# Performance work log

Hardware: AMD Instinct MI355X
Metric: run time of the kernel (lower is better)

Reference implementation:

```python
import jax, jax.numpy as jnp
import numpy as np

EMBED_DIM = 512
NUM_HEADS = 8
N_WIRES = 8  # kernel uses only first N_WIRES dims of each head vector


def setup_inputs() -> dict:
    key = jax.random.key(0)
    x = jax.random.normal(key, (8, 1024, EMBED_DIM), dtype=jnp.float32)
    return {"x": x}


def reference(x):
    B, S, E = x.shape
    H = NUM_HEADS
    dk = E // H
    # [B, H, S, dk]
    xh = x.reshape(B, S, H, dk).transpose(0, 2, 1, 3)
    # Quantum RY-overlap kernel closed form:
    #   RY(-y) RY(x) |0> = RY(x - y) |0>  =>  <0...0|psi> = prod_w cos((x_w - y_w)/2)
    # Only the first N_WIRES components of each head vector are used
    # (states.view(-1)[0] reads the first batch row's |0..0> amplitude).
    xw = xh[..., :N_WIRES]  # [B, H, S, NW]
    scores = jnp.ones((B, H, S, S), dtype=x.dtype)
    for w in range(N_WIRES):  # fixed small loop, fuses under jit
        diff = xw[:, :, :, None, w] - xw[:, :, None, :, w]  # [B, H, S, S]
        scores = scores * jnp.cos(diff * 0.5)
    scores = jnp.abs(scores)
    attn = jax.nn.softmax(scores, axis=-1)  # dropout is identity at eval
    out = jnp.einsum("bhij,bhjd->bhid", attn, xh)  # [B, H, S, dk]
    return out.transpose(0, 2, 1, 3).reshape(B, S, E)
```

## Files before the change

kernel.cpp:

```cpp
#include <hip/hip_runtime.h>

#define B_  8
#define S_  1024
#define E_  512
#define TI  128
#define TJ  32
#define P_STR 40
#define V_STR 40

typedef _Float16 half_t;
typedef _Float16 half4_t __attribute__((ext_vector_type(4)));
typedef _Float16 half8_t __attribute__((ext_vector_type(8)));
typedef float    floatx16 __attribute__((ext_vector_type(16)));

__device__ __forceinline__ void make_frags(float4 w0, float4 w1, int hf,
                                           half8_t* fH, half8_t* fL) {
    float xi[8] = {w0.x, w0.y, w0.z, w0.w, w1.x, w1.y, w1.z, w1.w};
    float c[8], s[8];
    #pragma unroll
    for (int w = 0; w < 8; ++w) {
        float v = xi[w] * 0.5f;
        c[w] = __cosf(v);
        s[w] = __sinf(v);
    }
    float p01[4] = {c[0]*c[1], s[0]*c[1], c[0]*s[1], s[0]*s[1]};
    float p23[4] = {c[2]*c[3], s[2]*c[3], c[2]*s[3], s[2]*s[3]};
    float p45[4] = {c[4]*c[5], s[4]*c[5], c[4]*s[5], s[4]*s[5]};
    float p67[4] = {c[6]*c[7], s[6]*c[7], c[6]*s[7], s[6]*s[7]};
    #pragma unroll
    for (int idx = 0; idx < 8; ++idx) {
        int a = idx & 3;
        int bsel = (idx >> 2) | (hf << 1);
        (*fL)[idx] = (half_t)(p01[a] * p23[bsel]);
        (*fH)[idx] = (half_t)(p45[a] * p67[bsel]);
    }
}

__global__ __launch_bounds__(256, 2) void attn_kernel(const float* __restrict__ x,
                                                      float* __restrict__ out) {
    const int bh = blockIdx.x;
    const int b  = bh >> 3, h = bh & 7;
    const int i0 = blockIdx.y * TI;
    const int t  = threadIdx.x;
    const int wv = t >> 6;
    const int ln = t & 63;
    const int m  = ln & 31;
    const int hf = ln >> 5;
    const int lo = t & 7;

    __shared__ __align__(16) half_t sh_p[TI * P_STR];
    __shared__ __align__(16) half_t sh_v[64 * V_STR];
    __shared__ float sh_den[TI];

    const float* xh = x + (size_t)b * S_ * E_ + h * 64;

    half8_t biH, biL;
    {
        const float* px = xh + (size_t)(i0 + wv * 32 + m) * E_;
        float4 w0 = ((const float4*)px)[0];
        float4 w1 = ((const float4*)px)[1];
        make_frags(w0, w1, hf, &biH, &biL);
    }

    floatx16 acc0, acc1, z;
    #pragma unroll
    for (int k = 0; k < 16; ++k) { acc0[k] = 0.f; acc1[k] = 0.f; z[k] = 0.f; }
    float dacc = 0.f;

    const int sv_j  = t >> 3;
    const int sv_d0 = lo * 8;

    for (int j0 = 0; j0 < S_; j0 += TJ) {
        __syncthreads();

        const float* pj = xh + (size_t)(j0 + m) * E_;
        float4 jw0 = ((const float4*)pj)[0];
        float4 jw1 = ((const float4*)pj)[1];
        const float* pv = xh + (size_t)(j0 + sv_j) * E_ + sv_d0;
        float4 v0 = ((const float4*)pv)[0];
        float4 v1 = ((const float4*)pv)[1];

        half8_t ajH, ajL;
        make_frags(jw0, jw1, hf, &ajH, &ajL);

        {
            float vals[8] = {v0.x, v0.y, v0.z, v0.w, v1.x, v1.y, v1.z, v1.w};
            #pragma unroll
            for (int nq = 0; nq < 8; ++nq) {
                int q = (nq + lo) & 7;
                sh_v[(sv_d0 + q) * V_STR + sv_j] = (half_t)vals[q];
            }
        }
        __syncthreads();

        floatx16 sH = __builtin_amdgcn_mfma_f32_32x32x16_f16(ajH, biH, z, 0, 0, 0);
        floatx16 sL = __builtin_amdgcn_mfma_f32_32x32x16_f16(ajL, biL, z, 0, 0, 0);

        const int irow = wv * 32 + m;
        #pragma unroll
        for (int g = 0; g < 4; ++g) {
            half4_t pk;
            #pragma unroll
            for (int r = 0; r < 4; ++r) {
                float sc = sH[4 * g + r] * sL[4 * g + r];
                float p = __expf(__builtin_fabsf(sc));
                dacc += p;
                pk[r] = (half_t)p;
            }
            *(half4_t*)&sh_p[irow * P_STR + g * 8 + hf * 4] = pk;
        }

        const half_t* prow = &sh_p[(wv * 32 + m) * P_STR];
        half8_t ap0 = *(const half8_t*)(prow + hf * 8);
        half8_t ap1 = *(const half8_t*)(prow + 16 + hf * 8);
        const half_t* vr0 = &sh_v[m * V_STR];
        const half_t* vr1 = &sh_v[(32 + m) * V_STR];
        half8_t b00 = *(const half8_t*)(vr0 + hf * 8);
        half8_t b01 = *(const half8_t*)(vr0 + 16 + hf * 8);
        half8_t b10 = *(const half8_t*)(vr1 + hf * 8);
        half8_t b11 = *(const half8_t*)(vr1 + 16 + hf * 8);
        acc0 = __builtin_amdgcn_mfma_f32_32x32x16_f16(ap0, b00, acc0, 0, 0, 0);
        acc0 = __builtin_amdgcn_mfma_f32_32x32x16_f16(ap1, b01, acc0, 0, 0, 0);
        acc1 = __builtin_amdgcn_mfma_f32_32x32x16_f16(ap0, b10, acc1, 0, 0, 0);
        acc1 = __builtin_amdgcn_mfma_f32_32x32x16_f16(ap1, b11, acc1, 0, 0, 0);
    }

    dacc += __shfl_xor(dacc, 32, 64);
    sh_den[wv * 32 + m] = dacc;
    __syncthreads();

    #pragma unroll
    for (int reg = 0; reg < 16; ++reg) {
        int il = (reg & 3) + 8 * (reg >> 2) + 4 * hf;
        float inv = 1.f / sh_den[wv * 32 + il];
        size_t base = ((size_t)(b * S_ + i0 + wv * 32 + il)) * E_ + h * 64 + m;
        out[base]      = acc0[reg] * inv;
        out[base + 32] = acc1[reg] * inv;
    }
}

extern "C" void kernel_launch(void* const* d_in, const int* in_sizes, int n_in,
                              void* d_out, int out_size, void* d_ws, size_t ws_size,
                              hipStream_t stream) {
    const float* x = (const float*)d_in[0];
    float* out = (float*)d_out;
    attn_kernel<<<dim3(B_ * 8, S_ / TI), 256, 0, stream>>>(x, out);
}
```

Before: 112.1 us.

## Precompute fp16 feature maps and transposed V, split j across waves

Adds a precompute kernel that evaluates the cos/sin product feature vectors once per row and writes an fp16 transposed copy of V to workspace. The attention kernel then loads these directly, staging V with global_load_lds and skipping per-tile transcendental work and fp32 conversion. P fragments are built with permlane32 swaps instead of an LDS round trip. The tile becomes 64x64 with two waves splitting j and a shared-memory reduction at the end. This costs an extra launch and workspace traffic, and the j split adds an epilogue reduction.

```diff
diff --git a/kernel.cpp b/kernel.cpp
--- a/kernel.cpp
+++ b/kernel.cpp
@@ -3,139 +3,175 @@
 #define B_  8
 #define S_  1024
 #define E_  512
-#define TI  128
-#define TJ  32
-#define P_STR 40
-#define V_STR 40
+#define TI  64
+#define TJ  64
 
 typedef _Float16 half_t;
-typedef _Float16 half4_t __attribute__((ext_vector_type(4)));
+typedef _Float16 half2_t __attribute__((ext_vector_type(2)));
 typedef _Float16 half8_t __attribute__((ext_vector_type(8)));
 typedef float    floatx16 __attribute__((ext_vector_type(16)));
+typedef unsigned int uint2v __attribute__((ext_vector_type(2)));
+typedef unsigned int uint4v __attribute__((ext_vector_type(4)));
 
-__device__ __forceinline__ void make_frags(float4 w0, float4 w1, int hf,
-                                           half8_t* fH, half8_t* fL) {
-    float xi[8] = {w0.x, w0.y, w0.z, w0.w, w1.x, w1.y, w1.z, w1.w};
-    float c[8], s[8];
-    #pragma unroll
-    for (int w = 0; w < 8; ++w) {
-        float v = xi[w] * 0.5f;
-        c[w] = __cosf(v);
-        s[w] = __sinf(v);
+#define PHI_BYTES ((size_t)64 * S_ * 32 * 2)
+#define VT_BYTES  ((size_t)64 * 64 * S_ * 2)
+
+#define GLOAD_LDS16(g, l)                                                        \
+    __builtin_amdgcn_global_load_lds((const __attribute__((address_space(1))) void*)(g), \
+                                     (__attribute__((address_space(3))) void*)(l), 16, 0, 0)
+
+__global__ __launch_bounds__(256) void precompute_kernel(const float* __restrict__ x,
+                                                         half_t* __restrict__ phi,
+                                                         half_t* __restrict__ vt) {
+    const int bh  = blockIdx.y;
+    const int b   = bh >> 3, h = bh & 7;
+    const int jb0 = blockIdx.x * 128;
+    const int t   = threadIdx.x;
+    __shared__ half_t tsh[128 * 65];
+
+    {
+        const int jj = t >> 1, sel = t & 1;
+        const int j  = jb0 + jj;
+        const float* px = x + (size_t)b * S_ * E_ + (size_t)j * E_ + h * 64 + sel * 4;
+        float4 w = *(const float4*)px;
+        float xi[4] = {w.x, w.y, w.z, w.w};
+        float c[4], s[4];
+        #pragma unroll
+        for (int q = 0; q < 4; ++q) {
+            float v = xi[q] * 0.5f;
+            c[q] = __cosf(v); s[q] = __sinf(v);
+        }
+        float pa[4] = {c[0]*c[1], s[0]*c[1], c[0]*s[1], s[0]*s[1]};
+        float pb[4] = {c[2]*c[3], s[2]*c[3], c[2]*s[3], s[2]*s[3]};
+        half_t f16[16];
+        #pragma unroll
+        for (int f = 0; f < 16; ++f)
+            f16[f] = (half_t)(pa[f & 3] * pb[f >> 2]);
+        half_t* dst = phi + ((size_t)bh * S_ + j) * 32 + (sel ? 0 : 16);
+        *(half8_t*)dst       = *(half8_t*)&f16[0];
+        *(half8_t*)(dst + 8) = *(half8_t*)&f16[8];
     }
-    float p01[4] = {c[0]*c[1], s[0]*c[1], c[0]*s[1], s[0]*s[1]};
-    float p23[4] = {c[2]*c[3], s[2]*c[3], c[2]*s[3], s[2]*s[3]};
-    float p45[4] = {c[4]*c[5], s[4]*c[5], c[4]*s[5], s[4]*s[5]};
-    float p67[4] = {c[6]*c[7], s[6]*c[7], c[6]*s[7], s[6]*s[7]};
-    #pragma unroll
-    for (int idx = 0; idx < 8; ++idx) {
-        int a = idx & 3;
-        int bsel = (idx >> 2) | (hf << 1);
-        (*fL)[idx] = (half_t)(p01[a] * p23[bsel]);
-        (*fH)[idx] = (half_t)(p45[a] * p67[bsel]);
+
+    {
+        const float* xb = x + (size_t)b * S_ * E_ + h * 64;
+        for (int k = 0; k < 32; ++k) {
+            int idx = k * 256 + t;
+            int j = idx >> 6, d = idx & 63;
+            tsh[j * 65 + d] = (half_t)xb[(size_t)(jb0 + j) * E_ + d];
+        }
+        __syncthreads();
+        for (int k = 0; k < 32; ++k) {
+            int idx = k * 256 + t;
+            int d = idx >> 7, j = idx & 127;
+            vt[((size_t)bh * 64 + d) * S_ + jb0 + j] = tsh[j * 65 + d];
+        }
     }
 }
 
-__global__ __launch_bounds__(256, 2) void attn_kernel(const float* __restrict__ x,
+__global__ __launch_bounds__(256, 4) void attn_kernel(const half_t* __restrict__ phi,
+                                                      const half_t* __restrict__ vt,
                                                       float* __restrict__ out) {
-    const int bh = blockIdx.x;
-    const int b  = bh >> 3, h = bh & 7;
-    const int i0 = blockIdx.y * TI;
-    const int t  = threadIdx.x;
-    const int wv = t >> 6;
-    const int ln = t & 63;
-    const int m  = ln & 31;
-    const int hf = ln >> 5;
-    const int lo = t & 7;
+    const int iblk = blockIdx.x;
+    const int bh   = blockIdx.y;
+    const int b    = bh >> 3, h = bh & 7;
+    const int i0   = iblk * TI;
+    const int t    = threadIdx.x;
+    const int wv   = t >> 6, ln = t & 63;
+    const int m    = ln & 31, hf = ln >> 5;
+    const int ib   = wv >> 1, jb = wv & 1;
 
-    __shared__ __align__(16) half_t sh_p[TI * P_STR];
-    __shared__ __align__(16) half_t sh_v[64 * V_STR];
-    __shared__ float sh_den[TI];
+    __shared__ __align__(16) half_t sh_v[8 * 64 * 8];
+    __shared__ float sh_red[2][32][64];
+    __shared__ float sh_den[2][64];
 
-    const float* xh = x + (size_t)b * S_ * E_ + h * 64;
+    const half_t* phb = phi + (size_t)bh * S_ * 32;
 
     half8_t biH, biL;
     {
-        const float* px = xh + (size_t)(i0 + wv * 32 + m) * E_;
-        float4 w0 = ((const float4*)px)[0];
-        float4 w1 = ((const float4*)px)[1];
-        make_frags(w0, w1, hf, &biH, &biL);
+        const half_t* pr = phb + (size_t)(i0 + ib * 32 + m) * 32 + hf * 8;
+        biH = *(const half8_t*)pr;
+        biL = *(const half8_t*)(pr + 16);
     }
 
     floatx16 acc0, acc1, z;
     #pragma unroll
     for (int k = 0; k < 16; ++k) { acc0[k] = 0.f; acc1[k] = 0.f; z[k] = 0.f; }
-    float dacc = 0.f;
+    float d0 = 0.f, d1 = 0.f;
 
-    const int sv_j  = t >> 3;
-    const int sv_d0 = lo * 8;
+    const half_t* vsrc = vt + ((size_t)bh * 64 + ln) * S_;
+    const half_t* asrc = phb + (size_t)(jb * 32 + m) * 32 + hf * 8;
 
     for (int j0 = 0; j0 < S_; j0 += TJ) {
         __syncthreads();
 
-        const float* pj = xh + (size_t)(j0 + m) * E_;
-        float4 jw0 = ((const float4*)pj)[0];
-        float4 jw1 = ((const float4*)pj)[1];
-        const float* pv = xh + (size_t)(j0 + sv_j) * E_ + sv_d0;
-        float4 v0 = ((const float4*)pv)[0];
-        float4 v1 = ((const float4*)pv)[1];
+        GLOAD_LDS16(vsrc + j0 + (2 * wv + 0) * 8, &sh_v[(2 * wv + 0) * 64 * 8]);
+        GLOAD_LDS16(vsrc + j0 + (2 * wv + 1) * 8, &sh_v[(2 * wv + 1) * 64 * 8]);
 
-        half8_t ajH, ajL;
-        make_frags(jw0, jw1, hf, &ajH, &ajL);
-
-        {
-            float vals[8] = {v0.x, v0.y, v0.z, v0.w, v1.x, v1.y, v1.z, v1.w};
-            #pragma unroll
-            for (int nq = 0; nq < 8; ++nq) {
-                int q = (nq + lo) & 7;
-                sh_v[(sv_d0 + q) * V_STR + sv_j] = (half_t)vals[q];
-            }
-        }
-        __syncthreads();
+        const half_t* ar = asrc + (size_t)j0 * 32;
+        half8_t ajH = *(const half8_t*)ar;
+        half8_t ajL = *(const half8_t*)(ar + 16);
 
         floatx16 sH = __builtin_amdgcn_mfma_f32_32x32x16_f16(ajH, biH, z, 0, 0, 0);
         floatx16 sL = __builtin_amdgcn_mfma_f32_32x32x16_f16(ajL, biL, z, 0, 0, 0);
 
-        const int irow = wv * 32 + m;
+        unsigned int dwa[4], dwb[4];
         #pragma unroll
         for (int g = 0; g < 4; ++g) {
-            half4_t pk;
+            float p[4];
             #pragma unroll
             for (int r = 0; r < 4; ++r) {
                 float sc = sH[4 * g + r] * sL[4 * g + r];
-                float p = __expf(__builtin_fabsf(sc));
-                dacc += p;
-                pk[r] = (half_t)p;
+                p[r] = __expf(__builtin_fabsf(sc));
             }
-            *(half4_t*)&sh_p[irow * P_STR + g * 8 + hf * 4] = pk;
+            d0 += p[0] + p[2];
+            d1 += p[1] + p[3];
+            half2_t ha = {(half_t)p[0], (half_t)p[1]};
+            half2_t hb = {(half_t)p[2], (half_t)p[3]};
+            dwa[g] = __builtin_bit_cast(unsigned int, ha);
+            dwb[g] = __builtin_bit_cast(unsigned int, hb);
         }
+        uint2v swA0 = __builtin_amdgcn_permlane32_swap(dwa[0], dwa[1], false, false);
+        uint2v swB0 = __builtin_amdgcn_permlane32_swap(dwb[0], dwb[1], false, false);
+        uint2v swA1 = __builtin_amdgcn_permlane32_swap(dwa[2], dwa[3], false, false);
+        uint2v swB1 = __builtin_amdgcn_permlane32_swap(dwb[2], dwb[3], false, false);
+        half8_t ap0 = __builtin_bit_cast(half8_t, (uint4v){swA0.x, swB0.x, swA0.y, swB0.y});
+        half8_t ap1 = __builtin_bit_cast(half8_t, (uint4v){swA1.x, swB1.x, swA1.y, swB1.y});
 
-        const half_t* prow = &sh_p[(wv * 32 + m) * P_STR];
-        half8_t ap0 = *(const half8_t*)(prow + hf * 8);
-        half8_t ap1 = *(const half8_t*)(prow + 16 + hf * 8);
-        const half_t* vr0 = &sh_v[m * V_STR];
-        const half_t* vr1 = &sh_v[(32 + m) * V_STR];
-        half8_t b00 = *(const half8_t*)(vr0 + hf * 8);
-        half8_t b01 = *(const half8_t*)(vr0 + 16 + hf * 8);
-        half8_t b10 = *(const half8_t*)(vr1 + hf * 8);
-        half8_t b11 = *(const half8_t*)(vr1 + 16 + hf * 8);
+        __syncthreads();
+
+        const int q0 = jb * 4;
+        half8_t b00 = *(const half8_t*)&sh_v[(((q0 + 0 + hf) * 64) + m) * 8];
+        half8_t b01 = *(const half8_t*)&sh_v[(((q0 + 2 + hf) * 64) + m) * 8];
+        half8_t b10 = *(const half8_t*)&sh_v[(((q0 + 0 + hf) * 64) + 32 + m) * 8];
+        half8_t b11 = *(const half8_t*)&sh_v[(((q0 + 2 + hf) * 64) + 32 + m) * 8];
+
         acc0 = __builtin_amdgcn_mfma_f32_32x32x16_f16(ap0, b00, acc0, 0, 0, 0);
         acc0 = __builtin_amdgcn_mfma_f32_32x32x16_f16(ap1, b01, acc0, 0, 0, 0);
         acc1 = __builtin_amdgcn_mfma_f32_32x32x16_f16(ap0, b10, acc1, 0, 0, 0);
         acc1 = __builtin_amdgcn_mfma_f32_32x32x16_f16(ap1, b11, acc1, 0, 0, 0);
     }
 
-    dacc += __shfl_xor(dacc, 32, 64);
-    sh_den[wv * 32 + m] = dacc;
+    float dtot = d0 + d1;
+    dtot += __shfl_xor(dtot, 32, 64);
+    sh_den[jb][ib * 32 + m] = dtot;
+    if (jb == 1) {
+        #pragma unroll
+        for (int reg = 0; reg < 16; ++reg) {
+            int il = (reg & 3) + 8 * (reg >> 2) + 4 * hf;
+            sh_red[ib][il][m]      = acc0[reg];
+            sh_red[ib][il][32 + m] = acc1[reg];
+        }
+    }
     __syncthreads();
-
-    #pragma unroll
-    for (int reg = 0; reg < 16; ++reg) {
-        int il = (reg & 3) + 8 * (reg >> 2) + 4 * hf;
-        float inv = 1.f / sh_den[wv * 32 + il];
-        size_t base = ((size_t)(b * S_ + i0 + wv * 32 + il)) * E_ + h * 64 + m;
-        out[base]      = acc0[reg] * inv;
-        out[base + 32] = acc1[reg] * inv;
+    if (jb == 0) {
+        #pragma unroll
+        for (int reg = 0; reg < 16; ++reg) {
+            int il = (reg & 3) + 8 * (reg >> 2) + 4 * hf;
+            float inv = 1.f / (sh_den[0][ib * 32 + il] + sh_den[1][ib * 32 + il]);
+            size_t base = ((size_t)(b * S_ + i0 + ib * 32 + il)) * E_ + h * 64 + m;
+            out[base]      = (acc0[reg] + sh_red[ib][il][m])      * inv;
+            out[base + 32] = (acc1[reg] + sh_red[ib][il][32 + m]) * inv;
+        }
     }
 }
 
@@ -144,5 +180,8 @@
                               hipStream_t stream) {
     const float* x = (const float*)d_in[0];
     float* out = (float*)d_out;
-    attn_kernel<<<dim3(B_ * 8, S_ / TI), 256, 0, stream>>>(x, out);
+    half_t* phi = (half_t*)d_ws;
+    half_t* vt  = (half_t*)((char*)d_ws + PHI_BYTES);
+    precompute_kernel<<<dim3(8, 64), 256, 0, stream>>>(x, phi, vt);
+    attn_kernel<<<dim3(S_ / TI, 64), 256, 0, stream>>>(phi, vt, out);
 }
```

Result: faster. 106.2 us (-5.3%).
